# Optimization experiments

Hardware: AMD Instinct MI355X
Metric: run time of the kernel (lower is better)

Reference implementation:

```python
import jax, jax.numpy as jnp
import numpy as np

N_HEADS = 16
EPS = 1e-5

def _ln(h, g, b):
    mu = jnp.mean(h, axis=-1, keepdims=True)
    var = jnp.var(h, axis=-1, keepdims=True)
    return (h - mu) * jax.lax.rsqrt(var + EPS) * g + b

def setup_inputs() -> dict:
    key = jax.random.key(0)
    ks = jax.random.split(key, 8)
    B, S, D, M = 2, 2048, 2048, 8192
    x = jax.random.normal(ks[0], (B, S, D), dtype=jnp.float32)
    # causal mask: True where attention is disallowed (j > i)
    mask = jnp.triu(jnp.ones((S, S), dtype=bool), k=1)[None, None]
    s = 1.0 / np.sqrt(D)
    Wq = jax.random.normal(ks[1], (D, D), dtype=jnp.float32) * s
    Wk = jax.random.normal(ks[2], (D, D), dtype=jnp.float32) * s
    Wv = jax.random.normal(ks[3], (D, D), dtype=jnp.float32) * s
    Wo = jax.random.normal(ks[4], (D, D), dtype=jnp.float32) * s
    W1 = jax.random.normal(ks[5], (D, M), dtype=jnp.float32) * s
    b1 = jnp.zeros((M,), dtype=jnp.float32)
    W2 = jax.random.normal(ks[6], (M, D), dtype=jnp.float32) * (1.0 / np.sqrt(M))
    b2 = jnp.zeros((D,), dtype=jnp.float32)
    ln1_g = jnp.ones((D,), jnp.float32); ln1_b = jnp.zeros((D,), jnp.float32)
    ln2_g = jnp.ones((D,), jnp.float32); ln2_b = jnp.zeros((D,), jnp.float32)
    return dict(x=x, self_attn_mask=mask, Wq=Wq, Wk=Wk, Wv=Wv, Wo=Wo,
                ln1_g=ln1_g, ln1_b=ln1_b, W1=W1, b1=b1, W2=W2, b2=b2,
                ln2_g=ln2_g, ln2_b=ln2_b)

def reference(x, self_attn_mask, Wq, Wk, Wv, Wo, ln1_g, ln1_b, W1, b1, W2, b2, ln2_g, ln2_b):
    B, S, D = x.shape
    n = N_HEADS
    d = D // n
    # --- self-attention with pre-norm residual ---
    h = _ln(x, ln1_g, ln1_b)
    # NOTE: source uses .view(b, n_heads, i, head_dim) with NO transpose -> plain reshape
    q = (h @ Wq).reshape(B, n, S, d)
    k = (h @ Wk).reshape(B, n, S, d)
    v = (h @ Wv).reshape(B, n, S, d)
    score = jnp.einsum('bnid,bnjd->bnij', q, k)
    # NOTE: source masks BEFORE scaling, so -1e9 is also divided by sqrt(d)
    score = jnp.where(self_attn_mask, jnp.float32(-1e9), score) / jnp.sqrt(jnp.float32(d))
    w = jax.nn.softmax(score, axis=3)
    o = jnp.einsum('bnij,bnjd->bnid', w, v)
    o = o.transpose(0, 2, 1, 3).reshape(B, S, D)  # b n i d -> b i (n d)
    x = x + o @ Wo
    # --- FFN with pre-norm residual ---
    h2 = _ln(x, ln2_g, ln2_b)
    ff = jnp.maximum(h2 @ W1 + b1, 0.0) @ W2 + b2
    return x + ff
```

## Files before the change

kernel.cpp:

```cpp
#include <hip/hip_runtime.h>
#include <cstdint>

using bf16x8 = __attribute__((ext_vector_type(8))) short;
using f32x4  = __attribute__((ext_vector_type(4))) float;

__device__ __forceinline__ unsigned short f2bf(float f) {
  union { float f; unsigned u; } v; v.f = f;
  unsigned u = v.u;
  u += 0x7fffu + ((u >> 16) & 1u);
  return (unsigned short)(u >> 16);
}

__device__ __forceinline__ void gload_lds16(const unsigned short* g, unsigned short* l) {
  __builtin_amdgcn_global_load_lds(
      (const __attribute__((address_space(1))) unsigned int*)g,
      (__attribute__((address_space(3))) unsigned int*)l, 16, 0, 0);
}

__global__ __launch_bounds__(256) void ln_kernel(
    const float* __restrict__ x, const float* __restrict__ g,
    const float* __restrict__ bb, unsigned short* __restrict__ h)
{
  const int D = 2048;
  const int row = blockIdx.x;
  const float* xr = x + (size_t)row * D;
  const int t = threadIdx.x;
  float4 v0 = ((const float4*)xr)[t];
  float4 v1 = ((const float4*)xr)[t + 256];
  float s  = v0.x+v0.y+v0.z+v0.w + v1.x+v1.y+v1.z+v1.w;
  float ss = v0.x*v0.x+v0.y*v0.y+v0.z*v0.z+v0.w*v0.w
           + v1.x*v1.x+v1.y*v1.y+v1.z*v1.z+v1.w*v1.w;
  #pragma unroll
  for (int off = 1; off < 64; off <<= 1) {
    s  += __shfl_xor(s, off);
    ss += __shfl_xor(ss, off);
  }
  __shared__ float red[8];
  const int wave = t >> 6, lane = t & 63;
  if (lane == 0) { red[wave] = s; red[4+wave] = ss; }
  __syncthreads();
  s  = red[0]+red[1]+red[2]+red[3];
  ss = red[4]+red[5]+red[6]+red[7];
  const float mu   = s * (1.f/2048.f);
  const float var  = ss * (1.f/2048.f) - mu*mu;
  const float rstd = rsqrtf(var + 1e-5f);
  unsigned short* hr = h + (size_t)row * D;
  #pragma unroll
  for (int q = 0; q < 2; ++q) {
    float4 v = q ? v1 : v0;
    int vecidx = t + q*256;
    float4 gg  = ((const float4*)g)[vecidx];
    float4 bv  = ((const float4*)bb)[vecidx];
    ushort4 o;
    o.x = f2bf((v.x-mu)*rstd*gg.x + bv.x);
    o.y = f2bf((v.y-mu)*rstd*gg.y + bv.y);
    o.z = f2bf((v.z-mu)*rstd*gg.z + bv.z);
    o.w = f2bf((v.w-mu)*rstd*gg.w + bv.w);
    *(ushort4*)(hr + vecidx*4) = o;
  }
}

__global__ __launch_bounds__(256) void transpose_cast(
    const float* __restrict__ W, unsigned short* __restrict__ WT,
    int K, int N)
{
  __shared__ float tile[32][33];
  const int tx = threadIdx.x, ty = threadIdx.y;
  const int n0 = blockIdx.x * 32, k0 = blockIdx.y * 32;
  #pragma unroll
  for (int r = 0; r < 4; ++r)
    tile[ty + r*8][tx] = W[(size_t)(k0 + ty + r*8) * N + n0 + tx];
  __syncthreads();
  #pragma unroll
  for (int r = 0; r < 4; ++r)
    WT[(size_t)(n0 + ty + r*8) * K + k0 + tx] = f2bf(tile[tx][ty + r*8]);
}

__global__ __launch_bounds__(256) void reduce_splitk(
    const float* __restrict__ P, const float* __restrict__ x2,
    const float* __restrict__ b2, float* __restrict__ out)
{
  const size_t MN4 = (size_t)4096 * 2048 / 4;
  const float4* P0 = (const float4*)P;
  const float4* P1 = P0 + MN4;
  const float4* X  = (const float4*)x2;
  const float4* B  = (const float4*)b2;
  for (size_t i = (size_t)blockIdx.x * 256 + threadIdx.x; i < MN4;
       i += (size_t)gridDim.x * 256) {
    float4 a = P0[i], b = P1[i], c = X[i], bb = B[i & 511];
    float4 o;
    o.x = a.x + b.x + c.x + bb.x;
    o.y = a.y + b.y + c.y + bb.y;
    o.z = a.z + b.z + c.z + bb.z;
    o.w = a.w + b.w + c.w + bb.w;
    ((float4*)out)[i] = o;
  }
}

template<int BM, bool BIAS, bool RELU, bool RESID, bool OUTBF16>
__global__ __launch_bounds__(512, 2) void gemm8(
    const unsigned short* __restrict__ A, const unsigned short* __restrict__ BT,
    const float* __restrict__ bias, const float* __restrict__ resid,
    void* __restrict__ Cp, int M, int N, int K, int kdepth, int nbx, int ntiles)
{
  constexpr int BN = 256, BK = 64;
  constexpr int MPH = BM / 64;
  constexpr int AQ  = BM / 64;
  constexpr int LPK = AQ + 4;
  __shared__ __align__(16) unsigned short lds[2][(BM + BN) * BK];

  const int tid  = threadIdx.x;
  const int lane = tid & 63, wave = tid >> 6;
  const int l15 = lane & 15, lh = lane >> 4;
  const int wr = wave >> 2, wc = wave & 3;

  const int nwg = gridDim.x;
  const int q8  = nwg >> 3;
  const int wg  = blockIdx.x;
  const int swz = (wg & 7) * q8 + (wg >> 3);
  const int split = swz / ntiles;
  const int tile  = swz % ntiles;
  const size_t bm = (size_t)(tile / nbx) * BM;
  const size_t bn = (size_t)(tile % nbx) * BN;
  A  += (size_t)split * kdepth;
  BT += (size_t)split * kdepth;
  const int nk = kdepth >> 6;

  auto stageA = [&](int buf, int kt, int qq) {
    int idx = qq * 512 + tid;
    int row = idx >> 3, c = idx & 7, gc = c ^ (row & 7);
    gload_lds16(A + (bm + row) * (size_t)K + (size_t)kt * BK + gc * 8,
                &lds[buf][0] + idx * 8);
  };
  auto stageB = [&](int buf, int kt, int qq) {
    int idx = qq * 512 + tid;
    int row = idx >> 3, c = idx & 7, gc = c ^ (row & 7);
    gload_lds16(BT + (bn + row) * (size_t)K + (size_t)kt * BK + gc * 8,
                &lds[buf][BM * BK] + idx * 8);
  };

  f32x4 acc[MPH * 2][4] = {};

  #pragma unroll
  for (int qq = 0; qq < AQ; ++qq) stageA(0, 0, qq);
  #pragma unroll
  for (int qq = 0; qq < 4; ++qq)  stageB(0, 0, qq);
  #pragma unroll
  for (int qq = 0; qq < AQ; ++qq) stageA(1, 1, qq);
  #pragma unroll
  for (int qq = 0; qq < 4; ++qq)  stageB(1, 1, qq);

  for (int kt = 0; kt < nk; ++kt) {
    const int buf = kt & 1;
    if (kt < nk - 1) asm volatile("s_waitcnt vmcnt(%0)" :: "i"(LPK) : "memory");
    else             asm volatile("s_waitcnt vmcnt(0)" ::: "memory");
    __builtin_amdgcn_s_barrier();
    asm volatile("" ::: "memory");

    const unsigned short* La = &lds[buf][0];
    const unsigned short* Lb = &lds[buf][BM * BK];
    const bool pf = (kt + 2 < nk);

    bf16x8 af[MPH][2][2];
    #pragma unroll
    for (int mi = 0; mi < 2; ++mi) {
      int arow = (wr * 2 + mi) * 16 + l15;
      #pragma unroll
      for (int kk = 0; kk < 2; ++kk)
        af[0][mi][kk] = *(const bf16x8*)(La + arow * 64 +
                          ((kk * 32 + lh * 8) ^ ((arow & 7) << 3)));
    }
    bf16x8 bfr[2][4];
    #pragma unroll
    for (int kk = 0; kk < 2; ++kk)
      #pragma unroll
      for (int n = 0; n < 4; ++n) {
        int brow = wc * 64 + n * 16 + l15;
        bfr[kk][n] = *(const bf16x8*)(Lb + brow * 64 +
                       ((kk * 32 + lh * 8) ^ ((brow & 7) << 3)));
      }

    #pragma unroll
    for (int p = 0; p < MPH; ++p) {
      if (p + 1 < MPH) {
        #pragma unroll
        for (int mi = 0; mi < 2; ++mi) {
          int arow = ((p + 1) * 4 + wr * 2 + mi) * 16 + l15;
          #pragma unroll
          for (int kk = 0; kk < 2; ++kk)
            af[p + 1][mi][kk] = *(const bf16x8*)(La + arow * 64 +
                                  ((kk * 32 + lh * 8) ^ ((arow & 7) << 3)));
        }
      }
      if (p > 0 && pf) {
        if (MPH == 4) { stageA(buf, kt + 2, p - 1); stageB(buf, kt + 2, p - 1); }
        else          { stageA(buf, kt + 2, 0);
                        stageB(buf, kt + 2, 0); stageB(buf, kt + 2, 1); }
      }
      __builtin_amdgcn_sched_barrier(0);
      __builtin_amdgcn_s_setprio(1);
      #pragma unroll
      for (int mi = 0; mi < 2; ++mi)
        #pragma unroll
        for (int n = 0; n < 4; ++n)
          #pragma unroll
          for (int kk = 0; kk < 2; ++kk)
            acc[p*2+mi][n] = __builtin_amdgcn_mfma_f32_16x16x32_bf16(
                af[p][mi][kk], bfr[kk][n], acc[p*2+mi][n], 0, 0, 0);
      __builtin_amdgcn_s_setprio(0);
      asm volatile("" ::: "memory");
      __builtin_amdgcn_s_barrier();
    }
    if (pf) {
      if (MPH == 4) { stageA(buf, kt + 2, 3); stageB(buf, kt + 2, 3); }
      else          { stageA(buf, kt + 2, 1);
                      stageB(buf, kt + 2, 2); stageB(buf, kt + 2, 3); }
    }
  }

  float bv[4];
  if (BIAS) {
    #pragma unroll
    for (int n = 0; n < 4; ++n) bv[n] = bias[bn + wc*64 + n*16 + l15];
  }
  unsigned short* Cb = (unsigned short*)Cp + (size_t)split * M * N;
  float*          Cf = (float*)Cp + (size_t)split * M * N;
  #pragma unroll
  for (int p = 0; p < MPH; ++p) {
    #pragma unroll
    for (int mi = 0; mi < 2; ++mi) {
      #pragma unroll
      for (int r = 0; r < 4; ++r) {
        size_t rrow = bm + (size_t)(p*4 + wr*2 + mi)*16 + lh*4 + r;
        #pragma unroll
        for (int n = 0; n < 4; ++n) {
          size_t ccol = bn + wc*64 + n*16 + l15;
          float v = acc[p*2+mi][n][r];
          if (BIAS)  v += bv[n];
          if (RELU)  v = fmaxf(v, 0.f);
          if (RESID) v += resid[rrow*(size_t)N + ccol];
          if (OUTBF16) Cb[rrow*(size_t)N + ccol] = f2bf(v);
          else         Cf[rrow*(size_t)N + ccol] = v;
        }
      }
    }
  }
}

__global__ __launch_bounds__(256) void attn_kernel(
    const unsigned short* __restrict__ QKV, unsigned short* __restrict__ O)
{
  constexpr float SCALE = 0.08838834764831845f;
  __shared__ __align__(16) unsigned short Kl[64*128];
  __shared__ __align__(16) unsigned short Vf[64*128];
  __shared__ __align__(16) unsigned short Pl[4*1024];
  const int bid = blockIdx.x;
  const int qt = 31 - (bid >> 5);
  const int nh = bid & 15;
  const int b  = (bid >> 4) & 1;
  const int t = threadIdx.x;
  const int lane = t & 63, wave = t >> 6;
  const int l15 = lane & 15, lh = lane >> 4;
  const int i0 = qt*64 + wave*16;
  const size_t RS = 6144;
  const size_t base = (size_t)b * 2048 * RS;

  const unsigned short* qrow = QKV + base + (size_t)(nh*128 + (i0 >> 4)) * RS;
  bf16x8 qf[4];
  #pragma unroll
  for (int c = 0; c < 4; ++c)
    qf[c] = *(const bf16x8*)(qrow + l15*128 + c*32 + lh*8);

  f32x4 of[8] = {};
  float mrun[4], lrun[4];
  #pragma unroll
  for (int r = 0; r < 4; ++r) { mrun[r] = -INFINITY; lrun[r] = 0.f; }

  const int nkt = qt + 1;
  bf16x8 kr[4], vr[4];
  auto loadKV = [&](int kt) {
    #pragma unroll
    for (int q = 0; q < 4; ++q) {
      int c = t + q*256;
      int j = c >> 4, dd0 = (c & 15) * 8;
      const size_t grow = base + (size_t)(nh*128 + kt*4 + (j >> 4)) * RS + (j & 15)*128 + dd0;
      kr[q] = *(const bf16x8*)(QKV + grow + 2048);
      vr[q] = *(const bf16x8*)(QKV + grow + 4096);
    }
  };
  loadKV(0);

  for (int kt = 0; kt < nkt; ++kt) {
    __syncthreads();
    #pragma unroll
    for (int q = 0; q < 4; ++q) {
      int c = t + q*256;
      int j = c >> 4, dd0 = (c & 15) * 8;
      *(bf16x8*)((char*)Kl + ((j*256 + dd0*2) ^ ((j & 7) << 4))) = kr[q];
      int ks = j >> 5, jq = j & 31;
      int cc = dd0 >> 4;
      int wb = ks*8192 + cc*1024 + (((dd0 & 15) + 16*((jq >> 3) & 3)) & ~7)*16 + (jq & 7)*2;
      #pragma unroll
      for (int e = 0; e < 8; ++e)
        *(unsigned short*)((char*)Vf + wb + ((e ^ cc) * 16)) = (unsigned short)vr[q][e];
    }
    __syncthreads();
    if (kt + 1 < nkt) loadKV(kt + 1);

    f32x4 sc[4] = {};
    #pragma unroll
    for (int jt = 0; jt < 4; ++jt) {
      int row = jt*16 + l15;
      const char* kb = (const char*)Kl + row*256;
      const int sw = (row & 7) << 4;
      #pragma unroll
      for (int c = 0; c < 4; ++c) {
        bf16x8 kf = *(const bf16x8*)(kb + ((c*64 + lh*16) ^ sw));
        sc[jt] = __builtin_amdgcn_mfma_f32_16x16x32_bf16(qf[c], kf, sc[jt], 0, 0, 0);
      }
    }

    float fac[4];
    char* pw = (char*)Pl + wave*2048;
    #pragma unroll
    for (int r = 0; r < 4; ++r) {
      float s0 = sc[0][r]*SCALE, s1 = sc[1][r]*SCALE, s2 = sc[2][r]*SCALE, s3 = sc[3][r]*SCALE;
      if (kt == qt) {
        const int i = i0 + lh*4 + r;
        const int j = kt*64 + l15;
        s0 = (j      > i) ? -INFINITY : s0;
        s1 = (j + 16 > i) ? -INFINITY : s1;
        s2 = (j + 32 > i) ? -INFINITY : s2;
        s3 = (j + 48 > i) ? -INFINITY : s3;
      }
      float mx = fmaxf(fmaxf(s0, s1), fmaxf(s2, s3));
      #pragma unroll
      for (int mk = 1; mk < 16; mk <<= 1) mx = fmaxf(mx, __shfl_xor(mx, mk));
      const float mnew = fmaxf(mrun[r], mx);
      float p0 = __expf(s0 - mnew), p1 = __expf(s1 - mnew);
      float p2 = __expf(s2 - mnew), p3 = __expf(s3 - mnew);
      float psum = (p0 + p1) + (p2 + p3);
      #pragma unroll
      for (int mk = 1; mk < 16; mk <<= 1) psum += __shfl_xor(psum, mk);
      fac[r]  = __expf(mrun[r] - mnew);
      lrun[r] = lrun[r]*fac[r] + psum;
      mrun[r] = mnew;
      const int io = lh*4 + r;
      const int swp = (io & 7) << 4;
      char* pr = pw + io*128;
      *(unsigned short*)(pr + ((     l15*2) ^ swp)) = f2bf(p0);
      *(unsigned short*)(pr + ((32 + l15*2) ^ swp)) = f2bf(p1);
      *(unsigned short*)(pr + ((64 + l15*2) ^ swp)) = f2bf(p2);
      *(unsigned short*)(pr + ((96 + l15*2) ^ swp)) = f2bf(p3);
    }
    #pragma unroll
    for (int c = 0; c < 8; ++c)
      #pragma unroll
      for (int r = 0; r < 4; ++r)
        of[c][r] *= fac[r];

    const char* prd = pw + l15*128;
    const int psw = (l15 & 7) << 4;
    bf16x8 pa0 = *(const bf16x8*)(prd + ((     lh*16) ^ psw));
    bf16x8 pa1 = *(const bf16x8*)(prd + ((64 + lh*16) ^ psw));

    #pragma unroll
    for (int c = 0; c < 8; ++c) {
      const char* vb = (const char*)Vf + c*1024 + ((lane ^ c) * 16);
      bf16x8 v0 = *(const bf16x8*)(vb);
      bf16x8 v1 = *(const bf16x8*)(vb + 8192);
      of[c] = __builtin_amdgcn_mfma_f32_16x16x32_bf16(pa0, v0, of[c], 0, 0, 0);
      of[c] = __builtin_amdgcn_mfma_f32_16x16x32_bf16(pa1, v1, of[c], 0, 0, 0);
    }
  }

  unsigned short* orow = O + ((size_t)(b*2048 + i0))*2048 + nh*128;
  #pragma unroll
  for (int r = 0; r < 4; ++r) {
    const float inv = 1.f / lrun[r];
    #pragma unroll
    for (int c = 0; c < 8; ++c)
      orow[(size_t)(lh*4 + r)*2048 + c*16 + l15] = f2bf(of[c][r]*inv);
  }
}

extern "C" void kernel_launch(void* const* d_in, const int* in_sizes, int n_in,
                              void* d_out, int out_size, void* d_ws, size_t ws_size,
                              hipStream_t stream)
{
  const float* x    = (const float*)d_in[0];
  const float* Wq   = (const float*)d_in[2];
  const float* Wk   = (const float*)d_in[3];
  const float* Wv   = (const float*)d_in[4];
  const float* Wo   = (const float*)d_in[5];
  const float* ln1g = (const float*)d_in[6];
  const float* ln1b = (const float*)d_in[7];
  const float* W1   = (const float*)d_in[8];
  const float* b1   = (const float*)d_in[9];
  const float* W2   = (const float*)d_in[10];
  const float* b2   = (const float*)d_in[11];
  const float* ln2g = (const float*)d_in[12];
  const float* ln2b = (const float*)d_in[13];
  float* out = (float*)d_out;

  char* ws = (char*)d_ws;
  unsigned short* WqkvT  = (unsigned short*)(ws);
  unsigned short* WoT    = (unsigned short*)(ws + 25165824);
  unsigned short* W1T    = (unsigned short*)(ws + 33554432);
  unsigned short* W2T    = (unsigned short*)(ws + 67108864);
  unsigned short* h      = (unsigned short*)(ws + 100663296);
  float*          x2     = (float*)(ws + 117440512);
  unsigned short* QKV    = (unsigned short*)(ws + 150994944);
  unsigned short* attn_o = (unsigned short*)(ws + 201326592);
  unsigned short* ff1    = (unsigned short*)(ws + 150994944);
  float*          Pws    = (float*)(ws);

  dim3 tb(32, 8);
  transpose_cast<<<dim3(64, 64),  tb, 0, stream>>>(Wq, WqkvT,                2048, 2048);
  transpose_cast<<<dim3(64, 64),  tb, 0, stream>>>(Wk, WqkvT + 2048*2048,    2048, 2048);
  transpose_cast<<<dim3(64, 64),  tb, 0, stream>>>(Wv, WqkvT + 2*2048*2048,  2048, 2048);
  transpose_cast<<<dim3(64, 64),  tb, 0, stream>>>(Wo, WoT,                  2048, 2048);
  transpose_cast<<<dim3(256, 64), tb, 0, stream>>>(W1, W1T,                  2048, 8192);
  transpose_cast<<<dim3(64, 256), tb, 0, stream>>>(W2, W2T,                  8192, 2048);

  ln_kernel<<<4096, 256, 0, stream>>>(x, ln1g, ln1b, h);
  gemm8<256,false,false,false,true><<<384, 512, 0, stream>>>(
      h, WqkvT, nullptr, nullptr, QKV, 4096, 6144, 2048, 2048, 24, 384);
  attn_kernel<<<1024, 256, 0, stream>>>(QKV, attn_o);
  gemm8<128,false,false,true,false><<<256, 512, 0, stream>>>(
      attn_o, WoT, nullptr, x, x2, 4096, 2048, 2048, 2048, 8, 256);
  ln_kernel<<<4096, 256, 0, stream>>>(x2, ln2g, ln2b, h);
  gemm8<256,true,true,false,true><<<512, 512, 0, stream>>>(
      h, W1T, b1, nullptr, ff1, 4096, 8192, 2048, 2048, 32, 512);
  gemm8<256,false,false,false,false><<<256, 512, 0, stream>>>(
      ff1, W2T, nullptr, nullptr, Pws, 4096, 2048, 8192, 4096, 8, 128);
  reduce_splitk<<<2048, 256, 0, stream>>>(Pws, x2, b2, out);
}
```

Baseline: 615.5 us.

## Use 128-row query tiles in attention and batch four weight transposes

The attention kernel now runs 8 waves per block over a 128-row query tile, so each staged K/V tile in LDS is shared by twice as many query rows and global K/V traffic is halved. Waves whose diagonal tile comes before the current key tile skip that compute, which adds some imbalance within a block. Separately, the four square weight transposes are merged into a single launch indexed by blockIdx.z, cutting launch overhead. Halving the grid to 512 blocks may lower parallelism for the causal load.

```diff
diff --git a/kernel.cpp b/kernel.cpp
--- a/kernel.cpp
+++ b/kernel.cpp
@@ -58,6 +58,24 @@
     o.w = f2bf((v.w-mu)*rstd*gg.w + bv.w);
     *(ushort4*)(hr + vecidx*4) = o;
   }
+}
+
+struct TPArgs { const float* src[4]; unsigned short* dst[4]; };
+__global__ __launch_bounds__(256) void transpose_cast4(TPArgs args)
+{
+  const float* W = args.src[blockIdx.z];
+  unsigned short* WT = args.dst[blockIdx.z];
+  const int K = 2048, N = 2048;
+  __shared__ float tile[32][33];
+  const int tx = threadIdx.x, ty = threadIdx.y;
+  const int n0 = blockIdx.x * 32, k0 = blockIdx.y * 32;
+  #pragma unroll
+  for (int r = 0; r < 4; ++r)
+    tile[ty + r*8][tx] = W[(size_t)(k0 + ty + r*8) * N + n0 + tx];
+  __syncthreads();
+  #pragma unroll
+  for (int r = 0; r < 4; ++r)
+    WT[(size_t)(n0 + ty + r*8) * K + k0 + tx] = f2bf(tile[tx][ty + r*8]);
 }
 
 __global__ __launch_bounds__(256) void transpose_cast(
@@ -114,9 +132,7 @@
   const int l15 = lane & 15, lh = lane >> 4;
   const int wr = wave >> 2, wc = wave & 3;
 
-  const int nwg = gridDim.x;
-  const int q8  = nwg >> 3;
-  const int wg  = blockIdx.x;
+  const int nwg = gridDim.x, q8 = nwg >> 3, wg = blockIdx.x;
   const int swz = (wg & 7) * q8 + (wg >> 3);
   const int split = swz / ntiles;
   const int tile  = swz % ntiles;
@@ -247,21 +263,22 @@
   }
 }
 
-__global__ __launch_bounds__(256) void attn_kernel(
+__global__ __launch_bounds__(512) void attn_kernel(
     const unsigned short* __restrict__ QKV, unsigned short* __restrict__ O)
 {
   constexpr float SCALE = 0.08838834764831845f;
   __shared__ __align__(16) unsigned short Kl[64*128];
   __shared__ __align__(16) unsigned short Vf[64*128];
-  __shared__ __align__(16) unsigned short Pl[4*1024];
+  __shared__ __align__(16) unsigned short Pl[8*1024];
   const int bid = blockIdx.x;
-  const int qt = 31 - (bid >> 5);
+  const int qtb = 15 - (bid >> 5);
   const int nh = bid & 15;
   const int b  = (bid >> 4) & 1;
   const int t = threadIdx.x;
   const int lane = t & 63, wave = t >> 6;
   const int l15 = lane & 15, lh = lane >> 4;
-  const int i0 = qt*64 + wave*16;
+  const int i0 = qtb*128 + wave*16;
+  const int dt = i0 >> 6;
   const size_t RS = 6144;
   const size_t base = (size_t)b * 2048 * RS;
 
@@ -276,12 +293,12 @@
   #pragma unroll
   for (int r = 0; r < 4; ++r) { mrun[r] = -INFINITY; lrun[r] = 0.f; }
 
-  const int nkt = qt + 1;
-  bf16x8 kr[4], vr[4];
+  const int nkt = 2*qtb + 2;
+  bf16x8 kr[2], vr[2];
   auto loadKV = [&](int kt) {
     #pragma unroll
-    for (int q = 0; q < 4; ++q) {
-      int c = t + q*256;
+    for (int q = 0; q < 2; ++q) {
+      int c = t + q*512;
       int j = c >> 4, dd0 = (c & 15) * 8;
       const size_t grow = base + (size_t)(nh*128 + kt*4 + (j >> 4)) * RS + (j & 15)*128 + dd0;
       kr[q] = *(const bf16x8*)(QKV + grow + 2048);
@@ -293,8 +310,8 @@
   for (int kt = 0; kt < nkt; ++kt) {
     __syncthreads();
     #pragma unroll
-    for (int q = 0; q < 4; ++q) {
-      int c = t + q*256;
+    for (int q = 0; q < 2; ++q) {
+      int c = t + q*512;
       int j = c >> 4, dd0 = (c & 15) * 8;
       *(bf16x8*)((char*)Kl + ((j*256 + dd0*2) ^ ((j & 7) << 4))) = kr[q];
       int ks = j >> 5, jq = j & 31;
@@ -307,70 +324,72 @@
     __syncthreads();
     if (kt + 1 < nkt) loadKV(kt + 1);
 
-    f32x4 sc[4] = {};
-    #pragma unroll
-    for (int jt = 0; jt < 4; ++jt) {
-      int row = jt*16 + l15;
-      const char* kb = (const char*)Kl + row*256;
-      const int sw = (row & 7) << 4;
-      #pragma unroll
-      for (int c = 0; c < 4; ++c) {
-        bf16x8 kf = *(const bf16x8*)(kb + ((c*64 + lh*16) ^ sw));
-        sc[jt] = __builtin_amdgcn_mfma_f32_16x16x32_bf16(qf[c], kf, sc[jt], 0, 0, 0);
-      }
-    }
-
-    float fac[4];
-    char* pw = (char*)Pl + wave*2048;
-    #pragma unroll
-    for (int r = 0; r < 4; ++r) {
-      float s0 = sc[0][r]*SCALE, s1 = sc[1][r]*SCALE, s2 = sc[2][r]*SCALE, s3 = sc[3][r]*SCALE;
-      if (kt == qt) {
-        const int i = i0 + lh*4 + r;
-        const int j = kt*64 + l15;
-        s0 = (j      > i) ? -INFINITY : s0;
-        s1 = (j + 16 > i) ? -INFINITY : s1;
-        s2 = (j + 32 > i) ? -INFINITY : s2;
-        s3 = (j + 48 > i) ? -INFINITY : s3;
-      }
-      float mx = fmaxf(fmaxf(s0, s1), fmaxf(s2, s3));
-      #pragma unroll
-      for (int mk = 1; mk < 16; mk <<= 1) mx = fmaxf(mx, __shfl_xor(mx, mk));
-      const float mnew = fmaxf(mrun[r], mx);
-      float p0 = __expf(s0 - mnew), p1 = __expf(s1 - mnew);
-      float p2 = __expf(s2 - mnew), p3 = __expf(s3 - mnew);
-      float psum = (p0 + p1) + (p2 + p3);
-      #pragma unroll
-      for (int mk = 1; mk < 16; mk <<= 1) psum += __shfl_xor(psum, mk);
-      fac[r]  = __expf(mrun[r] - mnew);
-      lrun[r] = lrun[r]*fac[r] + psum;
-      mrun[r] = mnew;
-      const int io = lh*4 + r;
-      const int swp = (io & 7) << 4;
-      char* pr = pw + io*128;
-      *(unsigned short*)(pr + ((     l15*2) ^ swp)) = f2bf(p0);
-      *(unsigned short*)(pr + ((32 + l15*2) ^ swp)) = f2bf(p1);
-      *(unsigned short*)(pr + ((64 + l15*2) ^ swp)) = f2bf(p2);
-      *(unsigned short*)(pr + ((96 + l15*2) ^ swp)) = f2bf(p3);
-    }
-    #pragma unroll
-    for (int c = 0; c < 8; ++c)
-      #pragma unroll
-      for (int r = 0; r < 4; ++r)
-        of[c][r] *= fac[r];
-
-    const char* prd = pw + l15*128;
-    const int psw = (l15 & 7) << 4;
-    bf16x8 pa0 = *(const bf16x8*)(prd + ((     lh*16) ^ psw));
-    bf16x8 pa1 = *(const bf16x8*)(prd + ((64 + lh*16) ^ psw));
-
-    #pragma unroll
-    for (int c = 0; c < 8; ++c) {
-      const char* vb = (const char*)Vf + c*1024 + ((lane ^ c) * 16);
-      bf16x8 v0 = *(const bf16x8*)(vb);
-      bf16x8 v1 = *(const bf16x8*)(vb + 8192);
-      of[c] = __builtin_amdgcn_mfma_f32_16x16x32_bf16(pa0, v0, of[c], 0, 0, 0);
-      of[c] = __builtin_amdgcn_mfma_f32_16x16x32_bf16(pa1, v1, of[c], 0, 0, 0);
+    if (kt <= dt) {
+      f32x4 sc[4] = {};
+      #pragma unroll
+      for (int jt = 0; jt < 4; ++jt) {
+        int row = jt*16 + l15;
+        const char* kb = (const char*)Kl + row*256;
+        const int sw = (row & 7) << 4;
+        #pragma unroll
+        for (int c = 0; c < 4; ++c) {
+          bf16x8 kf = *(const bf16x8*)(kb + ((c*64 + lh*16) ^ sw));
+          sc[jt] = __builtin_amdgcn_mfma_f32_16x16x32_bf16(qf[c], kf, sc[jt], 0, 0, 0);
+        }
+      }
+
+      float fac[4];
+      char* pw = (char*)Pl + wave*2048;
+      #pragma unroll
+      for (int r = 0; r < 4; ++r) {
+        float s0 = sc[0][r]*SCALE, s1 = sc[1][r]*SCALE, s2 = sc[2][r]*SCALE, s3 = sc[3][r]*SCALE;
+        if (kt == dt) {
+          const int i = i0 + lh*4 + r;
+          const int j = kt*64 + l15;
+          s0 = (j      > i) ? -INFINITY : s0;
+          s1 = (j + 16 > i) ? -INFINITY : s1;
+          s2 = (j + 32 > i) ? -INFINITY : s2;
+          s3 = (j + 48 > i) ? -INFINITY : s3;
+        }
+        float mx = fmaxf(fmaxf(s0, s1), fmaxf(s2, s3));
+        #pragma unroll
+        for (int mk = 1; mk < 16; mk <<= 1) mx = fmaxf(mx, __shfl_xor(mx, mk));
+        const float mnew = fmaxf(mrun[r], mx);
+        float p0 = __expf(s0 - mnew), p1 = __expf(s1 - mnew);
+        float p2 = __expf(s2 - mnew), p3 = __expf(s3 - mnew);
+        float psum = (p0 + p1) + (p2 + p3);
+        #pragma unroll
+        for (int mk = 1; mk < 16; mk <<= 1) psum += __shfl_xor(psum, mk);
+        fac[r]  = __expf(mrun[r] - mnew);
+        lrun[r] = lrun[r]*fac[r] + psum;
+        mrun[r] = mnew;
+        const int io = lh*4 + r;
+        const int swp = (io & 7) << 4;
+        char* pr = pw + io*128;
+        *(unsigned short*)(pr + ((     l15*2) ^ swp)) = f2bf(p0);
+        *(unsigned short*)(pr + ((32 + l15*2) ^ swp)) = f2bf(p1);
+        *(unsigned short*)(pr + ((64 + l15*2) ^ swp)) = f2bf(p2);
+        *(unsigned short*)(pr + ((96 + l15*2) ^ swp)) = f2bf(p3);
+      }
+      #pragma unroll
+      for (int c = 0; c < 8; ++c)
+        #pragma unroll
+        for (int r = 0; r < 4; ++r)
+          of[c][r] *= fac[r];
+
+      const char* prd = pw + l15*128;
+      const int psw = (l15 & 7) << 4;
+      bf16x8 pa0 = *(const bf16x8*)(prd + ((     lh*16) ^ psw));
+      bf16x8 pa1 = *(const bf16x8*)(prd + ((64 + lh*16) ^ psw));
+
+      #pragma unroll
+      for (int c = 0; c < 8; ++c) {
+        const char* vb = (const char*)Vf + c*1024 + ((lane ^ c) * 16);
+        bf16x8 v0 = *(const bf16x8*)(vb);
+        bf16x8 v1 = *(const bf16x8*)(vb + 8192);
+        of[c] = __builtin_amdgcn_mfma_f32_16x16x32_bf16(pa0, v0, of[c], 0, 0, 0);
+        of[c] = __builtin_amdgcn_mfma_f32_16x16x32_bf16(pa1, v1, of[c], 0, 0, 0);
+      }
     }
   }
 
@@ -416,17 +435,19 @@
   float*          Pws    = (float*)(ws);
 
   dim3 tb(32, 8);
-  transpose_cast<<<dim3(64, 64),  tb, 0, stream>>>(Wq, WqkvT,                2048, 2048);
-  transpose_cast<<<dim3(64, 64),  tb, 0, stream>>>(Wk, WqkvT + 2048*2048,    2048, 2048);
-  transpose_cast<<<dim3(64, 64),  tb, 0, stream>>>(Wv, WqkvT + 2*2048*2048,  2048, 2048);
-  transpose_cast<<<dim3(64, 64),  tb, 0, stream>>>(Wo, WoT,                  2048, 2048);
-  transpose_cast<<<dim3(256, 64), tb, 0, stream>>>(W1, W1T,                  2048, 8192);
-  transpose_cast<<<dim3(64, 256), tb, 0, stream>>>(W2, W2T,                  8192, 2048);
+  TPArgs tp;
+  tp.src[0] = Wq; tp.dst[0] = WqkvT;
+  tp.src[1] = Wk; tp.dst[1] = WqkvT + 2048*2048;
+  tp.src[2] = Wv; tp.dst[2] = WqkvT + 2*2048*2048;
+  tp.src[3] = Wo; tp.dst[3] = WoT;
+  transpose_cast4<<<dim3(64, 64, 4), tb, 0, stream>>>(tp);
+  transpose_cast<<<dim3(256, 64), tb, 0, stream>>>(W1, W1T, 2048, 8192);
+  transpose_cast<<<dim3(64, 256), tb, 0, stream>>>(W2, W2T, 8192, 2048);
 
   ln_kernel<<<4096, 256, 0, stream>>>(x, ln1g, ln1b, h);
   gemm8<256,false,false,false,true><<<384, 512, 0, stream>>>(
       h, WqkvT, nullptr, nullptr, QKV, 4096, 6144, 2048, 2048, 24, 384);
-  attn_kernel<<<1024, 256, 0, stream>>>(QKV, attn_o);
+  attn_kernel<<<512, 512, 0, stream>>>(QKV, attn_o);
   gemm8<128,false,false,true,false><<<256, 512, 0, stream>>>(
       attn_o, WoT, nullptr, x, x2, 4096, 2048, 2048, 2048, 8, 256);
   ln_kernel<<<4096, 256, 0, stream>>>(x2, ln2g, ln2b, h);
```

New measurement: 598.7 us, median of 3. 1.03x faster.
